# Performance work log

Measured on AMD Instinct MI355X. Metric: run time of the kernel, lower is better.

Reference implementation:

```python
import jax, jax.numpy as jnp
import numpy as np

N_NODES = 1_000_000
N_EDGES = 16_000_000


def setup_inputs() -> dict:
    key = jax.random.key(0)
    ks = jax.random.split(key, 8)
    x = jax.random.normal(ks[0], (N_NODES, 9), dtype=jnp.float32)
    edge_index = jax.random.randint(ks[1], (2, N_EDGES), 0, N_NODES, dtype=jnp.int64)
    # Glorot-ish scaled params
    W1 = jax.random.normal(ks[2], (9, 16), dtype=jnp.float32) * 0.3
    b1 = jax.random.normal(ks[3], (16,), dtype=jnp.float32) * 0.01
    W2 = jax.random.normal(ks[4], (16, 10), dtype=jnp.float32) * 0.25
    b2 = jax.random.normal(ks[5], (10,), dtype=jnp.float32) * 0.01
    Wf = jax.random.normal(ks[6], (10, 1), dtype=jnp.float32) * 0.3
    bf = jax.random.normal(ks[7], (1,), dtype=jnp.float32) * 0.01
    return {"x": x, "edge_index": edge_index, "W1": W1, "b1": b1,
            "W2": W2, "b2": b2, "Wf": Wf, "bf": bf}


def _gcn_conv(x, W, b, row, col, norm, n):
    # PyG GCNConv: linear transform, then normalized scatter-add aggregation.
    h = x @ W                                   # [N, out]
    msg = h[row] * norm[:, None]                # gather + edgewise scale [E+N, out]
    out = jax.ops.segment_sum(msg, col, num_segments=n)  # scatter-add [N, out]
    return out + b


def reference(x, edge_index, W1, b1, W2, b2, Wf, bf):
    n = x.shape[0]
    # add self-loops (PyG default add_self_loops=True)
    loop = jnp.arange(n, dtype=edge_index.dtype)
    row = jnp.concatenate([edge_index[0], loop])
    col = jnp.concatenate([edge_index[1], loop])
    # symmetric normalization: deg computed over target nodes, weight 1 per edge
    deg = jax.ops.segment_sum(jnp.ones(row.shape[0], dtype=x.dtype), col,
                              num_segments=n)
    deg_inv_sqrt = jnp.where(deg > 0, jax.lax.rsqrt(jnp.maximum(deg, 1.0)), 0.0)
    norm = deg_inv_sqrt[row] * deg_inv_sqrt[col]  # [E+N]

    h = _gcn_conv(x, W1, b1, row, col, norm, n)
    h = jax.nn.relu(h)
    # dropout is identity in eval mode
    h = _gcn_conv(h, W2, b2, row, col, norm, n)
    return h @ Wf + bf
```

## Files before the change

kernel.cpp:

```cpp
#include <hip/hip_runtime.h>

static constexpr int NN = 1000000;
static constexpr int NE = 16000000;
static constexpr int BSH = 11;
static constexpr int BNODES = 1 << BSH;
static constexpr int BMASK = BNODES - 1;
static constexpr int NB = (NN + BMASK) >> BSH;
static constexpr int NWG = 500;
static constexpr int EPW = NE / NWG;
static constexpr int CHUNK = 16;
static constexpr int CAP = 24;


__global__ __launch_bounds__(512) void k_count(const int* __restrict__ col,
                                               int* __restrict__ counts) {
    __shared__ int cnt[4][NB];
    for (int i = threadIdx.x; i < 4 * NB; i += 512) ((int*)cnt)[i] = 0;
    __syncthreads();
    int w = blockIdx.x;
    int rep = threadIdx.x & 3;
    const int4* col4 = (const int4*)(col + (long long)w * EPW);
    const int nq = EPW / 4;
    int q = threadIdx.x;
    for (; q + 512 < nq; q += 1024) {
        int4 a = col4[q];
        int4 b = col4[q + 512];
        atomicAdd(&cnt[rep][a.x >> BSH], 1);
        atomicAdd(&cnt[rep][a.y >> BSH], 1);
        atomicAdd(&cnt[rep][a.z >> BSH], 1);
        atomicAdd(&cnt[rep][a.w >> BSH], 1);
        atomicAdd(&cnt[rep][b.x >> BSH], 1);
        atomicAdd(&cnt[rep][b.y >> BSH], 1);
        atomicAdd(&cnt[rep][b.z >> BSH], 1);
        atomicAdd(&cnt[rep][b.w >> BSH], 1);
    }
    for (; q < nq; q += 512) {
        int4 a = col4[q];
        atomicAdd(&cnt[rep][a.x >> BSH], 1);
        atomicAdd(&cnt[rep][a.y >> BSH], 1);
        atomicAdd(&cnt[rep][a.z >> BSH], 1);
        atomicAdd(&cnt[rep][a.w >> BSH], 1);
    }
    __syncthreads();
    for (int i = threadIdx.x; i < NB; i += 512)
        counts[i * NWG + w] = cnt[0][i] + cnt[1][i] + cnt[2][i] + cnt[3][i];
}


__global__ __launch_bounds__(512) void k_scan_wg(int* __restrict__ counts,
                                                 int* __restrict__ bucketTotal) {
    __shared__ int sm[512];
    int b = blockIdx.x, t = threadIdx.x;
    int v = (t < NWG) ? counts[b * NWG + t] : 0;
    sm[t] = v;
    __syncthreads();
    for (int off = 1; off < 512; off <<= 1) {
        int x = (t >= off) ? sm[t - off] : 0;
        __syncthreads();
        sm[t] += x;
        __syncthreads();
    }
    if (t < NWG) counts[b * NWG + t] = sm[t] - v;
    if (t == 511) bucketTotal[b] = sm[511];
}


__global__ void k_scan_total(const int* __restrict__ bucketTotal,
                             int* __restrict__ bucketBase, int* __restrict__ ptr) {
    __shared__ int sm[512];
    int t = threadIdx.x;
    int v = (t < NB) ? bucketTotal[t] : 0;
    sm[t] = v;
    __syncthreads();
    for (int off = 1; off < 512; off <<= 1) {
        int x = (t >= off) ? sm[t - off] : 0;
        __syncthreads();
        sm[t] += x;
        __syncthreads();
    }
    if (t < NB) bucketBase[t] = sm[t] - v;
    if (t == 0) { bucketBase[NB] = NE; ptr[NN] = NE; }
}


__global__ __launch_bounds__(512) void k_bin2(const int* __restrict__ row,
                                              const int* __restrict__ col,
                                              const int* __restrict__ counts,
                                              const int* __restrict__ bucketBase,
                                              unsigned* __restrict__ binned) {
    __shared__ unsigned stage[NB][CAP];
    __shared__ int scnt[NB];
    __shared__ int gcur[NB];
    int w = blockIdx.x;
    for (int i = threadIdx.x; i < NB; i += 512) {
        scnt[i] = 0;
        gcur[i] = bucketBase[i] + counts[i * NWG + w];
    }
    __syncthreads();
    const int4* col4 = (const int4*)(col + (long long)w * EPW);
    const int4* row4 = (const int4*)(row + (long long)w * EPW);
    const int nq = EPW / 4;
    for (int q0 = 0; q0 < nq; q0 += 512) {
        int q = q0 + threadIdx.x;
        int4 c, r;
        bool ok = (q < nq);
        if (ok) { c = col4[q]; r = row4[q]; }
        if (ok) {
            int cc[4] = {c.x, c.y, c.z, c.w};
            int rr[4] = {r.x, r.y, r.z, r.w};
#pragma unroll
            for (int k = 0; k < 4; ++k) {
                int b = cc[k] >> BSH;
                unsigned v = ((unsigned)rr[k] << BSH) | (unsigned)(cc[k] & BMASK);
                int s = atomicAdd(&scnt[b], 1);
                if (s < CAP) stage[b][s] = v;
                else { int p = atomicAdd(&gcur[b], 1); binned[p] = v; }
            }
        }
        __syncthreads();
        for (int b = threadIdx.x; b < NB; b += 512) {
            int n = scnt[b]; if (n > CAP) n = CAP;
            if (n >= CHUNK) {
                int p = atomicAdd(&gcur[b], CHUNK);
#pragma unroll
                for (int t = 0; t < CHUNK; ++t) binned[p + t] = stage[b][t];
                int rem = n - CHUNK;
                for (int t = 0; t < rem; ++t) stage[b][t] = stage[b][CHUNK + t];
                scnt[b] = rem;
            } else {
                scnt[b] = n;
            }
        }
        __syncthreads();
    }
    for (int b = threadIdx.x; b < NB; b += 512) {
        int n = scnt[b]; if (n > CAP) n = CAP;
        if (n > 0) {
            int p = atomicAdd(&gcur[b], n);
            for (int t = 0; t < n; ++t) binned[p + t] = stage[b][t];
        }
    }
}


__global__ __launch_bounds__(512) void k_sort(const unsigned* __restrict__ binned,
                                              const int* __restrict__ bucketBase,
                                              const float* __restrict__ x,
                                              const float* __restrict__ W1,
                                              int* __restrict__ ptr,
                                              float* __restrict__ dis,
                                              int* __restrict__ sortedRow,
                                              float* __restrict__ g1) {
    __shared__ int cnt[BNODES];
    __shared__ int tsum[512];
    __shared__ float w1s[144];
    int b = blockIdx.x, t = threadIdx.x;
    if (t < 144) w1s[t] = W1[t];
    for (int i = t; i < BNODES; i += 512) cnt[i] = 0;
    __syncthreads();
    int i0 = bucketBase[b], i1 = bucketBase[b + 1];
    int i = i0 + t;
    for (; i + 3584 < i1; i += 4096) {
        unsigned v0 = binned[i],        v1 = binned[i +  512];
        unsigned v2 = binned[i + 1024], v3 = binned[i + 1536];
        unsigned v4 = binned[i + 2048], v5 = binned[i + 2560];
        unsigned v6 = binned[i + 3072], v7 = binned[i + 3584];
        atomicAdd(&cnt[v0 & BMASK], 1);
        atomicAdd(&cnt[v1 & BMASK], 1);
        atomicAdd(&cnt[v2 & BMASK], 1);
        atomicAdd(&cnt[v3 & BMASK], 1);
        atomicAdd(&cnt[v4 & BMASK], 1);
        atomicAdd(&cnt[v5 & BMASK], 1);
        atomicAdd(&cnt[v6 & BMASK], 1);
        atomicAdd(&cnt[v7 & BMASK], 1);
    }
    for (; i < i1; i += 512) atomicAdd(&cnt[binned[i] & BMASK], 1);
    __syncthreads();
    int s0 = cnt[t * 4], s1 = cnt[t * 4 + 1], s2 = cnt[t * 4 + 2], s3 = cnt[t * 4 + 3];
    int tot = s0 + s1 + s2 + s3;
    tsum[t] = tot;
    __syncthreads();
    for (int off = 1; off < 512; off <<= 1) {
        int x_ = (t >= off) ? tsum[t - off] : 0;
        __syncthreads();
        tsum[t] += x_;
        __syncthreads();
    }
    int base = bucketBase[b] + tsum[t] - tot;
    int n0 = (b << BSH) + t * 4;
    float d0 = rsqrtf((float)(s0 + 1)), d1 = rsqrtf((float)(s1 + 1));
    float d2 = rsqrtf((float)(s2 + 1)), d3 = rsqrtf((float)(s3 + 1));
    if (n0 < NN)     { ptr[n0]     = base;                dis[n0]     = d0; }
    if (n0 + 1 < NN) { ptr[n0 + 1] = base + s0;           dis[n0 + 1] = d1; }
    if (n0 + 2 < NN) { ptr[n0 + 2] = base + s0 + s1;      dis[n0 + 2] = d2; }
    if (n0 + 3 < NN) { ptr[n0 + 3] = base + s0 + s1 + s2; dis[n0 + 3] = d3; }
    __syncthreads();
    cnt[t * 4]     = base;
    cnt[t * 4 + 1] = base + s0;
    cnt[t * 4 + 2] = base + s0 + s1;
    cnt[t * 4 + 3] = base + s0 + s1 + s2;
    __syncthreads();
    i = i0 + t;
    for (; i + 3584 < i1; i += 4096) {
        unsigned v0 = binned[i],        v1 = binned[i +  512];
        unsigned v2 = binned[i + 1024], v3 = binned[i + 1536];
        unsigned v4 = binned[i + 2048], v5 = binned[i + 2560];
        unsigned v6 = binned[i + 3072], v7 = binned[i + 3584];
        int p0 = atomicAdd(&cnt[v0 & BMASK], 1);
        int p1 = atomicAdd(&cnt[v1 & BMASK], 1);
        int p2 = atomicAdd(&cnt[v2 & BMASK], 1);
        int p3 = atomicAdd(&cnt[v3 & BMASK], 1);
        int p4 = atomicAdd(&cnt[v4 & BMASK], 1);
        int p5 = atomicAdd(&cnt[v5 & BMASK], 1);
        int p6 = atomicAdd(&cnt[v6 & BMASK], 1);
        int p7 = atomicAdd(&cnt[v7 & BMASK], 1);
        sortedRow[p0] = (int)(v0 >> BSH);
        sortedRow[p1] = (int)(v1 >> BSH);
        sortedRow[p2] = (int)(v2 >> BSH);
        sortedRow[p3] = (int)(v3 >> BSH);
        sortedRow[p4] = (int)(v4 >> BSH);
        sortedRow[p5] = (int)(v5 >> BSH);
        sortedRow[p6] = (int)(v6 >> BSH);
        sortedRow[p7] = (int)(v7 >> BSH);
    }
    for (; i < i1; i += 512) {
        unsigned v = binned[i];
        int pos = atomicAdd(&cnt[v & BMASK], 1);
        sortedRow[pos] = (int)(v >> BSH);
    }
    float dd[4] = {d0, d1, d2, d3};
#pragma unroll
    for (int k = 0; k < 4; ++k) {
        int n = n0 + k;
        if (n >= NN) break;
        const float4* xp = (const float4*)(x + (long long)n * 9);
        const float* xs = x + (long long)n * 9;
        float xv[9];
#pragma unroll
        for (int m = 0; m < 9; ++m) xv[m] = xs[m];
        float d = dd[k];
        float o[16];
#pragma unroll
        for (int j = 0; j < 16; ++j) {
            float acc = 0.f;
#pragma unroll
            for (int m = 0; m < 9; ++m) acc = fmaf(xv[m], w1s[m * 16 + j], acc);
            o[j] = acc * d;
        }
        float4* dst = (float4*)(g1 + (long long)n * 16);
        dst[0] = make_float4(o[0], o[1], o[2], o[3]);
        dst[1] = make_float4(o[4], o[5], o[6], o[7]);
        dst[2] = make_float4(o[8], o[9], o[10], o[11]);
        dst[3] = make_float4(o[12], o[13], o[14], o[15]);
        (void)xp;
    }
}


template <int MODE>
__global__ void k_pull_f(const int* __restrict__ ptr, const int* __restrict__ sortedRow,
                         const float* __restrict__ dis, const float* __restrict__ g,
                         const float* __restrict__ p0, const float* __restrict__ p1,
                         const float* __restrict__ p2, float* __restrict__ dst) {
    __shared__ float w2s[256];
    __shared__ float c16[16];
    __shared__ float wf16[16];
    __shared__ float bfs;
    if (MODE == 0) {
        if (threadIdx.x < 256) {
            int k = threadIdx.x >> 4, j = threadIdx.x & 15;
            w2s[threadIdx.x] = (j < 10) ? p1[k * 10 + j] : 0.f;
        }
        if (threadIdx.x < 16) c16[threadIdx.x] = p0[threadIdx.x];
    } else {
        if (threadIdx.x < 16) {
            c16[threadIdx.x]  = (threadIdx.x < 10) ? p0[threadIdx.x] : 0.f;
            wf16[threadIdx.x] = (threadIdx.x < 10) ? p1[threadIdx.x] : 0.f;
        }
        if (threadIdx.x == 0) bfs = p2[0];
    }
    __syncthreads();

    int grp = threadIdx.x >> 4;
    int j = threadIdx.x & 15;
    int n = blockIdx.x * 16 + grp;
    if (n >= NN) return;
    int e0 = ptr[n], e1 = ptr[n + 1];
    float acc = g[(long long)n * 16 + j];
    int e = e0;
    for (; e + 16 <= e1; e += 16) {
        int r[16];
#pragma unroll
        for (int k = 0; k < 16; ++k) r[k] = sortedRow[e + k];
        float v[16];
#pragma unroll
        for (int k = 0; k < 16; ++k) v[k] = g[(long long)r[k] * 16 + j];
        float s0 = ((v[0] + v[1]) + (v[2] + v[3])) + ((v[4] + v[5]) + (v[6] + v[7]));
        float s1 = ((v[8] + v[9]) + (v[10] + v[11])) + ((v[12] + v[13]) + (v[14] + v[15]));
        acc += s0 + s1;
    }
    for (; e + 4 <= e1; e += 4) {
        int r0 = sortedRow[e + 0], r1 = sortedRow[e + 1];
        int r2 = sortedRow[e + 2], r3 = sortedRow[e + 3];
        float v0 = g[(long long)r0 * 16 + j];
        float v1 = g[(long long)r1 * 16 + j];
        float v2 = g[(long long)r2 * 16 + j];
        float v3 = g[(long long)r3 * 16 + j];
        acc += (v0 + v1) + (v2 + v3);
    }
    for (; e < e1; ++e)
        acc += g[(long long)sortedRow[e] * 16 + j];

    float d = dis[n];
    float val = d * acc;
    if (MODE == 0) {
        float hv = fmaxf(val + c16[j], 0.f);
        float o = 0.f;
#pragma unroll
        for (int k = 0; k < 16; ++k)
            o = fmaf(__shfl(hv, k, 16), w2s[k * 16 + j], o);
        dst[(long long)n * 16 + j] = o * d;
    } else {
        float t = (val + c16[j]) * wf16[j];
#pragma unroll
        for (int m = 8; m >= 1; m >>= 1) t += __shfl_xor(t, m, 16);
        if (j == 0) dst[n] = t + bfs;
    }
}

extern "C" void kernel_launch(void* const* d_in, const int* in_sizes, int n_in,
                              void* d_out, int out_size, void* d_ws, size_t ws_size,
                              hipStream_t stream) {
    const float* x  = (const float*)d_in[0];
    const int*   ei = (const int*)d_in[1];
    const float* W1 = (const float*)d_in[2];
    const float* b1 = (const float*)d_in[3];
    const float* W2 = (const float*)d_in[4];
    const float* b2 = (const float*)d_in[5];
    const float* Wf = (const float*)d_in[6];
    const float* bf = (const float*)d_in[7];
    float* out = (float*)d_out;

    const int* row = ei;
    const int* col = ei + NE;

    char* ws = (char*)d_ws;
    size_t off = 0;
    auto alloc = [&](size_t bytes) -> void* {
        void* p = ws + off;
        off += (bytes + 255) & ~255ULL;
        return p;
    };
    int* counts      = (int*)alloc((size_t)NB * NWG * 4);
    int* bucketTotal = (int*)alloc((size_t)NB * 4);
    int* bucketBase  = (int*)alloc((size_t)(NB + 1) * 4);
    int* ptr         = (int*)alloc((size_t)(NN + 1) * 4);
    float* dis       = (float*)alloc((size_t)NN * 4);
    unsigned* binned = (unsigned*)alloc((size_t)NE * 4);
    int* sortedRow   = (int*)alloc((size_t)NE * 4);
    float* g1        = (float*)alloc((size_t)NN * 16 * 4);

    float* g2 = (float*)binned;

    const int TB = 256;
    const int pullGrid = (NN + 15) / 16;

    k_count<<<NWG, 512, 0, stream>>>(col, counts);
    k_scan_wg<<<NB, 512, 0, stream>>>(counts, bucketTotal);
    k_scan_total<<<1, 512, 0, stream>>>(bucketTotal, bucketBase, ptr);
    k_bin2<<<NWG, 512, 0, stream>>>(row, col, counts, bucketBase, binned);
    k_sort<<<NB, 512, 0, stream>>>(binned, bucketBase, x, W1, ptr, dis, sortedRow, g1);

    k_pull_f<0><<<pullGrid, TB, 0, stream>>>(ptr, sortedRow, dis, g1, b1, W2, nullptr, g2);
    k_pull_f<1><<<pullGrid, TB, 0, stream>>>(ptr, sortedRow, dis, g2, b2, Wf, bf, out);
}
```

Measured before the change: 876.2 us.

## Replace count-and-scan prepass with fixed-capacity padded buckets using sentinels

Removes the separate counting pass over col and the two prefix-scan kernels. Each bucket now gets a fixed-capacity region, and binning appends 16-element chunks via a global atomic cursor, padding partial chunks with sentinel values and tracking the pad count. The sort kernel skips sentinels, and bucket bases are computed afterwards from fill minus padding. This saves one full read of the column array but enlarges the binned buffer and adds sentinel writes and reads. It also assumes no bucket overflows CAPB.

```diff
diff --git a/kernel.cpp b/kernel.cpp
--- a/kernel.cpp
+++ b/kernel.cpp
@@ -6,96 +6,29 @@
 static constexpr int BNODES = 1 << BSH;
 static constexpr int BMASK = BNODES - 1;
 static constexpr int NB = (NN + BMASK) >> BSH;
+static constexpr int CAPB = 43008;
 static constexpr int NWG = 500;
 static constexpr int EPW = NE / NWG;
 static constexpr int CHUNK = 16;
 static constexpr int CAP = 24;
-
-
-__global__ __launch_bounds__(512) void k_count(const int* __restrict__ col,
-                                               int* __restrict__ counts) {
-    __shared__ int cnt[4][NB];
-    for (int i = threadIdx.x; i < 4 * NB; i += 512) ((int*)cnt)[i] = 0;
-    __syncthreads();
-    int w = blockIdx.x;
-    int rep = threadIdx.x & 3;
-    const int4* col4 = (const int4*)(col + (long long)w * EPW);
-    const int nq = EPW / 4;
-    int q = threadIdx.x;
-    for (; q + 512 < nq; q += 1024) {
-        int4 a = col4[q];
-        int4 b = col4[q + 512];
-        atomicAdd(&cnt[rep][a.x >> BSH], 1);
-        atomicAdd(&cnt[rep][a.y >> BSH], 1);
-        atomicAdd(&cnt[rep][a.z >> BSH], 1);
-        atomicAdd(&cnt[rep][a.w >> BSH], 1);
-        atomicAdd(&cnt[rep][b.x >> BSH], 1);
-        atomicAdd(&cnt[rep][b.y >> BSH], 1);
-        atomicAdd(&cnt[rep][b.z >> BSH], 1);
-        atomicAdd(&cnt[rep][b.w >> BSH], 1);
-    }
-    for (; q < nq; q += 512) {
-        int4 a = col4[q];
-        atomicAdd(&cnt[rep][a.x >> BSH], 1);
-        atomicAdd(&cnt[rep][a.y >> BSH], 1);
-        atomicAdd(&cnt[rep][a.z >> BSH], 1);
-        atomicAdd(&cnt[rep][a.w >> BSH], 1);
-    }
-    __syncthreads();
-    for (int i = threadIdx.x; i < NB; i += 512)
-        counts[i * NWG + w] = cnt[0][i] + cnt[1][i] + cnt[2][i] + cnt[3][i];
-}
-
-
-__global__ __launch_bounds__(512) void k_scan_wg(int* __restrict__ counts,
-                                                 int* __restrict__ bucketTotal) {
-    __shared__ int sm[512];
-    int b = blockIdx.x, t = threadIdx.x;
-    int v = (t < NWG) ? counts[b * NWG + t] : 0;
-    sm[t] = v;
-    __syncthreads();
-    for (int off = 1; off < 512; off <<= 1) {
-        int x = (t >= off) ? sm[t - off] : 0;
-        __syncthreads();
-        sm[t] += x;
-        __syncthreads();
-    }
-    if (t < NWG) counts[b * NWG + t] = sm[t] - v;
-    if (t == 511) bucketTotal[b] = sm[511];
-}
-
-
-__global__ void k_scan_total(const int* __restrict__ bucketTotal,
-                             int* __restrict__ bucketBase, int* __restrict__ ptr) {
-    __shared__ int sm[512];
-    int t = threadIdx.x;
-    int v = (t < NB) ? bucketTotal[t] : 0;
-    sm[t] = v;
-    __syncthreads();
-    for (int off = 1; off < 512; off <<= 1) {
-        int x = (t >= off) ? sm[t - off] : 0;
-        __syncthreads();
-        sm[t] += x;
-        __syncthreads();
-    }
-    if (t < NB) bucketBase[t] = sm[t] - v;
-    if (t == 0) { bucketBase[NB] = NE; ptr[NN] = NE; }
-}
-
-
-__global__ __launch_bounds__(512) void k_bin2(const int* __restrict__ row,
+static constexpr unsigned SENT = 0xFFFFFFFFu;
+
+
+__global__ void k_init(int* __restrict__ cur, int* __restrict__ padc) {
+    int i = blockIdx.x * blockDim.x + threadIdx.x;
+    if (i < NB) { cur[i] = 0; padc[i] = 0; }
+}
+
+
+__global__ __launch_bounds__(512) void k_bin3(const int* __restrict__ row,
                                               const int* __restrict__ col,
-                                              const int* __restrict__ counts,
-                                              const int* __restrict__ bucketBase,
+                                              int* __restrict__ cur,
+                                              int* __restrict__ padc,
                                               unsigned* __restrict__ binned) {
     __shared__ unsigned stage[NB][CAP];
     __shared__ int scnt[NB];
-    __shared__ int gcur[NB];
     int w = blockIdx.x;
-    for (int i = threadIdx.x; i < NB; i += 512) {
-        scnt[i] = 0;
-        gcur[i] = bucketBase[i] + counts[i * NWG + w];
-    }
+    for (int i = threadIdx.x; i < NB; i += 512) scnt[i] = 0;
     __syncthreads();
     const int4* col4 = (const int4*)(col + (long long)w * EPW);
     const int4* row4 = (const int4*)(row + (long long)w * EPW);
@@ -114,16 +47,24 @@
                 unsigned v = ((unsigned)rr[k] << BSH) | (unsigned)(cc[k] & BMASK);
                 int s = atomicAdd(&scnt[b], 1);
                 if (s < CAP) stage[b][s] = v;
-                else { int p = atomicAdd(&gcur[b], 1); binned[p] = v; }
+                else {
+                    int p = atomicAdd(&cur[b], CHUNK);
+                    unsigned* dst = binned + (long long)b * CAPB + p;
+                    dst[0] = v;
+#pragma unroll
+                    for (int t = 1; t < CHUNK; ++t) dst[t] = SENT;
+                    atomicAdd(&padc[b], CHUNK - 1);
+                }
             }
         }
         __syncthreads();
         for (int b = threadIdx.x; b < NB; b += 512) {
             int n = scnt[b]; if (n > CAP) n = CAP;
             if (n >= CHUNK) {
-                int p = atomicAdd(&gcur[b], CHUNK);
-#pragma unroll
-                for (int t = 0; t < CHUNK; ++t) binned[p + t] = stage[b][t];
+                int p = atomicAdd(&cur[b], CHUNK);
+                uint4* src = (uint4*)&stage[b][0];
+                uint4* dst = (uint4*)(binned + (long long)b * CAPB + p);
+                dst[0] = src[0]; dst[1] = src[1]; dst[2] = src[2]; dst[3] = src[3];
                 int rem = n - CHUNK;
                 for (int t = 0; t < rem; ++t) stage[b][t] = stage[b][CHUNK + t];
                 scnt[b] = rem;
@@ -136,14 +77,36 @@
     for (int b = threadIdx.x; b < NB; b += 512) {
         int n = scnt[b]; if (n > CAP) n = CAP;
         if (n > 0) {
-            int p = atomicAdd(&gcur[b], n);
-            for (int t = 0; t < n; ++t) binned[p + t] = stage[b][t];
-        }
-    }
+            int p = atomicAdd(&cur[b], CHUNK);
+            unsigned* dst = binned + (long long)b * CAPB + p;
+            for (int t = 0; t < n; ++t) dst[t] = stage[b][t];
+            for (int t = n; t < CHUNK; ++t) dst[t] = SENT;
+            atomicAdd(&padc[b], CHUNK - n);
+        }
+    }
+}
+
+
+__global__ void k_bbase(const int* __restrict__ cur, const int* __restrict__ padc,
+                        int* __restrict__ bucketBase, int* __restrict__ ptr) {
+    __shared__ int sm[512];
+    int t = threadIdx.x;
+    int v = (t < NB) ? (cur[t] - padc[t]) : 0;
+    sm[t] = v;
+    __syncthreads();
+    for (int off = 1; off < 512; off <<= 1) {
+        int x = (t >= off) ? sm[t - off] : 0;
+        __syncthreads();
+        sm[t] += x;
+        __syncthreads();
+    }
+    if (t < NB) bucketBase[t] = sm[t] - v;
+    if (t == 0) { bucketBase[NB] = NE; ptr[NN] = NE; }
 }
 
 
 __global__ __launch_bounds__(512) void k_sort(const unsigned* __restrict__ binned,
+                                              const int* __restrict__ cur,
                                               const int* __restrict__ bucketBase,
                                               const float* __restrict__ x,
                                               const float* __restrict__ W1,
@@ -158,23 +121,30 @@
     if (t < 144) w1s[t] = W1[t];
     for (int i = t; i < BNODES; i += 512) cnt[i] = 0;
     __syncthreads();
-    int i0 = bucketBase[b], i1 = bucketBase[b + 1];
-    int i = i0 + t;
-    for (; i + 3584 < i1; i += 4096) {
-        unsigned v0 = binned[i],        v1 = binned[i +  512];
-        unsigned v2 = binned[i + 1024], v3 = binned[i + 1536];
-        unsigned v4 = binned[i + 2048], v5 = binned[i + 2560];
-        unsigned v6 = binned[i + 3072], v7 = binned[i + 3584];
-        atomicAdd(&cnt[v0 & BMASK], 1);
-        atomicAdd(&cnt[v1 & BMASK], 1);
-        atomicAdd(&cnt[v2 & BMASK], 1);
-        atomicAdd(&cnt[v3 & BMASK], 1);
-        atomicAdd(&cnt[v4 & BMASK], 1);
-        atomicAdd(&cnt[v5 & BMASK], 1);
-        atomicAdd(&cnt[v6 & BMASK], 1);
-        atomicAdd(&cnt[v7 & BMASK], 1);
-    }
-    for (; i < i1; i += 512) atomicAdd(&cnt[binned[i] & BMASK], 1);
+    long long B0 = (long long)b * CAPB;
+    int fill = cur[b];
+    {
+        long long i = B0 + t;
+        long long i1 = B0 + fill;
+        for (; i + 3584 < i1; i += 4096) {
+            unsigned v0 = binned[i],        v1 = binned[i +  512];
+            unsigned v2 = binned[i + 1024], v3 = binned[i + 1536];
+            unsigned v4 = binned[i + 2048], v5 = binned[i + 2560];
+            unsigned v6 = binned[i + 3072], v7 = binned[i + 3584];
+            if (v0 != SENT) atomicAdd(&cnt[v0 & BMASK], 1);
+            if (v1 != SENT) atomicAdd(&cnt[v1 & BMASK], 1);
+            if (v2 != SENT) atomicAdd(&cnt[v2 & BMASK], 1);
+            if (v3 != SENT) atomicAdd(&cnt[v3 & BMASK], 1);
+            if (v4 != SENT) atomicAdd(&cnt[v4 & BMASK], 1);
+            if (v5 != SENT) atomicAdd(&cnt[v5 & BMASK], 1);
+            if (v6 != SENT) atomicAdd(&cnt[v6 & BMASK], 1);
+            if (v7 != SENT) atomicAdd(&cnt[v7 & BMASK], 1);
+        }
+        for (; i < i1; i += 512) {
+            unsigned v = binned[i];
+            if (v != SENT) atomicAdd(&cnt[v & BMASK], 1);
+        }
+    }
     __syncthreads();
     int s0 = cnt[t * 4], s1 = cnt[t * 4 + 1], s2 = cnt[t * 4 + 2], s3 = cnt[t * 4 + 3];
     int tot = s0 + s1 + s2 + s3;
@@ -200,40 +170,33 @@
     cnt[t * 4 + 2] = base + s0 + s1;
     cnt[t * 4 + 3] = base + s0 + s1 + s2;
     __syncthreads();
-    i = i0 + t;
-    for (; i + 3584 < i1; i += 4096) {
-        unsigned v0 = binned[i],        v1 = binned[i +  512];
-        unsigned v2 = binned[i + 1024], v3 = binned[i + 1536];
-        unsigned v4 = binned[i + 2048], v5 = binned[i + 2560];
-        unsigned v6 = binned[i + 3072], v7 = binned[i + 3584];
-        int p0 = atomicAdd(&cnt[v0 & BMASK], 1);
-        int p1 = atomicAdd(&cnt[v1 & BMASK], 1);
-        int p2 = atomicAdd(&cnt[v2 & BMASK], 1);
-        int p3 = atomicAdd(&cnt[v3 & BMASK], 1);
-        int p4 = atomicAdd(&cnt[v4 & BMASK], 1);
-        int p5 = atomicAdd(&cnt[v5 & BMASK], 1);
-        int p6 = atomicAdd(&cnt[v6 & BMASK], 1);
-        int p7 = atomicAdd(&cnt[v7 & BMASK], 1);
-        sortedRow[p0] = (int)(v0 >> BSH);
-        sortedRow[p1] = (int)(v1 >> BSH);
-        sortedRow[p2] = (int)(v2 >> BSH);
-        sortedRow[p3] = (int)(v3 >> BSH);
-        sortedRow[p4] = (int)(v4 >> BSH);
-        sortedRow[p5] = (int)(v5 >> BSH);
-        sortedRow[p6] = (int)(v6 >> BSH);
-        sortedRow[p7] = (int)(v7 >> BSH);
-    }
-    for (; i < i1; i += 512) {
-        unsigned v = binned[i];
-        int pos = atomicAdd(&cnt[v & BMASK], 1);
-        sortedRow[pos] = (int)(v >> BSH);
+    {
+        long long i = B0 + t;
+        long long i1 = B0 + fill;
+        for (; i + 3584 < i1; i += 4096) {
+            unsigned v0 = binned[i],        v1 = binned[i +  512];
+            unsigned v2 = binned[i + 1024], v3 = binned[i + 1536];
+            unsigned v4 = binned[i + 2048], v5 = binned[i + 2560];
+            unsigned v6 = binned[i + 3072], v7 = binned[i + 3584];
+            if (v0 != SENT) sortedRow[atomicAdd(&cnt[v0 & BMASK], 1)] = (int)(v0 >> BSH);
+            if (v1 != SENT) sortedRow[atomicAdd(&cnt[v1 & BMASK], 1)] = (int)(v1 >> BSH);
+            if (v2 != SENT) sortedRow[atomicAdd(&cnt[v2 & BMASK], 1)] = (int)(v2 >> BSH);
+            if (v3 != SENT) sortedRow[atomicAdd(&cnt[v3 & BMASK], 1)] = (int)(v3 >> BSH);
+            if (v4 != SENT) sortedRow[atomicAdd(&cnt[v4 & BMASK], 1)] = (int)(v4 >> BSH);
+            if (v5 != SENT) sortedRow[atomicAdd(&cnt[v5 & BMASK], 1)] = (int)(v5 >> BSH);
+            if (v6 != SENT) sortedRow[atomicAdd(&cnt[v6 & BMASK], 1)] = (int)(v6 >> BSH);
+            if (v7 != SENT) sortedRow[atomicAdd(&cnt[v7 & BMASK], 1)] = (int)(v7 >> BSH);
+        }
+        for (; i < i1; i += 512) {
+            unsigned v = binned[i];
+            if (v != SENT) sortedRow[atomicAdd(&cnt[v & BMASK], 1)] = (int)(v >> BSH);
+        }
     }
     float dd[4] = {d0, d1, d2, d3};
 #pragma unroll
     for (int k = 0; k < 4; ++k) {
         int n = n0 + k;
         if (n >= NN) break;
-        const float4* xp = (const float4*)(x + (long long)n * 9);
         const float* xs = x + (long long)n * 9;
         float xv[9];
 #pragma unroll
@@ -252,7 +215,6 @@
         dst[1] = make_float4(o[4], o[5], o[6], o[7]);
         dst[2] = make_float4(o[8], o[9], o[10], o[11]);
         dst[3] = make_float4(o[12], o[13], o[14], o[15]);
-        (void)xp;
     }
 }
 
@@ -351,12 +313,12 @@
         off += (bytes + 255) & ~255ULL;
         return p;
     };
-    int* counts      = (int*)alloc((size_t)NB * NWG * 4);
-    int* bucketTotal = (int*)alloc((size_t)NB * 4);
+    int* cur         = (int*)alloc((size_t)NB * 4);
+    int* padc        = (int*)alloc((size_t)NB * 4);
     int* bucketBase  = (int*)alloc((size_t)(NB + 1) * 4);
     int* ptr         = (int*)alloc((size_t)(NN + 1) * 4);
     float* dis       = (float*)alloc((size_t)NN * 4);
-    unsigned* binned = (unsigned*)alloc((size_t)NE * 4);
+    unsigned* binned = (unsigned*)alloc((size_t)NB * CAPB * 4);
     int* sortedRow   = (int*)alloc((size_t)NE * 4);
     float* g1        = (float*)alloc((size_t)NN * 16 * 4);
 
@@ -365,11 +327,10 @@
     const int TB = 256;
     const int pullGrid = (NN + 15) / 16;
 
-    k_count<<<NWG, 512, 0, stream>>>(col, counts);
-    k_scan_wg<<<NB, 512, 0, stream>>>(counts, bucketTotal);
-    k_scan_total<<<1, 512, 0, stream>>>(bucketTotal, bucketBase, ptr);
-    k_bin2<<<NWG, 512, 0, stream>>>(row, col, counts, bucketBase, binned);
-    k_sort<<<NB, 512, 0, stream>>>(binned, bucketBase, x, W1, ptr, dis, sortedRow, g1);
+    k_init<<<(NB + 255) / 256, 256, 0, stream>>>(cur, padc);
+    k_bin3<<<NWG, 512, 0, stream>>>(row, col, cur, padc, binned);
+    k_bbase<<<1, 512, 0, stream>>>(cur, padc, bucketBase, ptr);
+    k_sort<<<NB, 512, 0, stream>>>(binned, cur, bucketBase, x, W1, ptr, dis, sortedRow, g1);
 
     k_pull_f<0><<<pullGrid, TB, 0, stream>>>(ptr, sortedRow, dis, g1, b1, W2, nullptr, g2);
     k_pull_f<1><<<pullGrid, TB, 0, stream>>>(ptr, sortedRow, dis, g2, b2, Wf, bf, out);
```

Measured after the change: 962.2 us. 9.8% more time.
